# Optimization experiments

Measured on AMD Instinct MI355X. Metric: run time of the kernel, lower is better.

The kernel has to match this reference:

```python
import jax, jax.numpy as jnp
import numpy as np

D_MODEL = 1024
N_HEADS = 16
HEAD_DIM = D_MODEL // N_HEADS
NEG = -10000.0  # module uses -10000, not -inf


def setup_inputs() -> dict:
    key = jax.random.key(0)
    ks = jax.random.split(key, 8)
    B, T = 4, 2048
    q = jax.random.normal(ks[0], (B, T, D_MODEL), dtype=jnp.float32)
    k = jax.random.normal(ks[1], (B, T, D_MODEL), dtype=jnp.float32)
    v = jax.random.normal(ks[2], (B, T, D_MODEL), dtype=jnp.float32)
    attn_mask = jnp.ones((B, T), dtype=jnp.float32)
    # xavier_uniform for square [d, d] weights: limit = sqrt(6/(d+d))
    lim = float(np.sqrt(6.0 / (D_MODEL + D_MODEL)))
    Wq = jax.random.uniform(ks[3], (D_MODEL, D_MODEL), jnp.float32, -lim, lim)
    Wk = jax.random.uniform(ks[4], (D_MODEL, D_MODEL), jnp.float32, -lim, lim)
    Wv = jax.random.uniform(ks[5], (D_MODEL, D_MODEL), jnp.float32, -lim, lim)
    Wo = jax.random.uniform(ks[6], (D_MODEL, D_MODEL), jnp.float32, -lim, lim)
    return {"q": q, "k": k, "v": v, "attn_mask": attn_mask,
            "Wq": Wq, "Wk": Wk, "Wv": Wv, "Wo": Wo, "mask_future": 1}


def _split_heads(x):
    B, T, _ = x.shape
    return x.reshape(B, T, N_HEADS, HEAD_DIM).transpose(0, 2, 1, 3)  # [B,H,T,D]


def reference(q, k, v, attn_mask, Wq, Wk, Wv, Wo, mask_future):
    # torch Linear: y = x @ W.T  (weights stored [out, in])
    qh = _split_heads(jnp.einsum('btd,ed->bte', q, Wq))
    kh = _split_heads(jnp.einsum('btd,ed->bte', k, Wk))
    vh = _split_heads(jnp.einsum('btd,ed->bte', v, Wv))
    L, S = qh.shape[-2], kh.shape[-2]
    # dual scale: each of q and k scaled by 1/d**0.25
    scale = 1.0 / jnp.sqrt(jnp.sqrt(jnp.float32(HEAD_DIM)))
    scores = jnp.einsum('bhld,bhsd->bhls', qh * scale, kh * scale)
    if mask_future:
        causal_bias = jnp.triu(jnp.full((L, S), NEG, dtype=scores.dtype), k=1)
        scores = scores + causal_bias
    # padding mask: attn_mask [B, S] -> broadcast [B,1,1,S]; 0 entries -> -10000
    pad = attn_mask[:, None, None, :]
    scores = jnp.where(pad == 0, jnp.asarray(NEG, scores.dtype), scores)
    probs = jax.nn.softmax(scores, axis=-1)  # dropout p=0.0 -> identity
    ctx = jnp.einsum('bhls,bhsd->bhld', probs, vh)
    B = ctx.shape[0]
    ctx = ctx.transpose(0, 2, 1, 3).reshape(B, L, D_MODEL)
    return jnp.einsum('btd,ed->bte', ctx, Wo)
```

## Files before the change

kernel.cpp:

```cpp
#include <hip/hip_runtime.h>

typedef unsigned short u16;
typedef __attribute__((ext_vector_type(8))) _Float16 f16x8;
typedef __attribute__((ext_vector_type(2))) __fp16 fp16v2;
typedef __attribute__((ext_vector_type(4))) float f32x4;
typedef __attribute__((ext_vector_type(16))) float f32x16;

#define T_SEQ 2048
#define NH 16
#define DH 64
#define DM 1024
#define NEG2 (-14426.95f)
#define QS2 (0.42466089f)

__device__ __forceinline__ unsigned pk2(float a, float b) {
  union { fp16v2 v; unsigned u; } c;
  c.v = __builtin_amdgcn_cvt_pkrtz(a, b);
  return c.u;
}
__device__ __forceinline__ u16 f2h(float a) {
  union { _Float16 h; u16 u; } c; c.h = (_Float16)a; return c.u;
}

__device__ __forceinline__ void async_load16(const void* g, void* l) {
  __builtin_amdgcn_global_load_lds(
      (const __attribute__((address_space(1))) unsigned int*)(g),
      (__attribute__((address_space(3))) unsigned int*)(l), 16, 0, 0);
}

__global__ __launch_bounds__(256) void convert_all(
    const float* __restrict__ q, const float* __restrict__ k, const float* __restrict__ v,
    const float* __restrict__ Wq, const float* __restrict__ Wk, const float* __restrict__ Wv,
    const float* __restrict__ Wo, u16* __restrict__ xb, u16* __restrict__ wb) {
  int blk = blockIdx.x;
  const float* src; u16* dst;
  if (blk < 12288) {
    int s = blk >> 12;
    src = (s == 0) ? q : (s == 1) ? k : v;
    dst = xb + (size_t)s * 8388608u;
    blk &= 4095;
  } else {
    int s = (blk - 12288) >> 9;
    src = (s == 0) ? Wq : (s == 1) ? Wk : (s == 2) ? Wv : Wo;
    dst = wb + (size_t)s * 1048576u;
    blk = (blk - 12288) & 511;
  }
  size_t base = (size_t)blk * 2048 + (size_t)threadIdx.x * 8;
  float4 a = *(const float4*)(src + base);
  float4 b2 = *(const float4*)(src + base + 4);
  uint4 st;
  st.x = pk2(a.x, a.y); st.y = pk2(a.z, a.w);
  st.z = pk2(b2.x, b2.y); st.w = pk2(b2.z, b2.w);
  *(uint4*)(dst + base) = st;
}

__global__ __launch_bounds__(256) void gemm_qkv(const u16* __restrict__ A,
                                                const u16* __restrict__ Wqb,
                                                const u16* __restrict__ Wkb,
                                                const u16* __restrict__ Wvb,
                                                u16* __restrict__ Qh, u16* __restrict__ Kh,
                                                u16* __restrict__ VTh) {
  __shared__ char lds[33792];
  const int tid = threadIdx.x;
  const int wid = tid >> 6, lane = tid & 63;
  const int l32 = lane & 31, lh = lane >> 5;
  const int m0 = blockIdx.x * 128;
  const int n0 = blockIdx.y * 128;
  const int which = n0 >> 10;
  const int n0l = n0 & 1023;
  const u16* As = A + (size_t)which * 8388608u;
  const u16* Bw = (which == 0) ? Wqb : (which == 1) ? Wkb : Wvb;
  const int wm = wid >> 1, wn = wid & 1;
  f32x16 acc[2][2] = {};

  const u16* gA = As + (size_t)(m0 + wid * 32 + l32) * 1024 + lh * 8;
  const u16* gB = Bw + (size_t)(n0l + wid * 32 + l32) * 1024 + lh * 8;
  async_load16(gA, lds + (wid * 2 + 0) * 1024);
  async_load16(gA + 16, lds + (wid * 2 + 1) * 1024);
  async_load16(gB, lds + 8192 + (wid * 2 + 0) * 1024);
  async_load16(gB + 16, lds + 8192 + (wid * 2 + 1) * 1024);

  for (int it = 0; it < 32; ++it) {
    __syncthreads();
    char* cur = lds + (it & 1) * 16384;
    if (it < 31) {
      char* nxt = lds + ((it + 1) & 1) * 16384;
      int kt = (it + 1) * 32;
      async_load16(gA + kt, nxt + (wid * 2 + 0) * 1024);
      async_load16(gA + kt + 16, nxt + (wid * 2 + 1) * 1024);
      async_load16(gB + kt, nxt + 8192 + (wid * 2 + 0) * 1024);
      async_load16(gB + kt + 16, nxt + 8192 + (wid * 2 + 1) * 1024);
    }
    char* const rb = (which < 2) ? (cur + 8192) : cur;
    char* const cb = (which < 2) ? cur : (cur + 8192);
    for (int ks = 0; ks < 2; ++ks) {
      f16x8 rf[2], cf[2];
      for (int i = 0; i < 2; ++i) {
        rf[i] = *(const f16x8*)(rb + ((wm * 2 + i) * 2 + ks) * 1024 + lane * 16);
        cf[i] = *(const f16x8*)(cb + ((wn * 2 + i) * 2 + ks) * 1024 + lane * 16);
      }
      for (int i = 0; i < 2; ++i)
        for (int j = 0; j < 2; ++j)
          acc[i][j] = __builtin_amdgcn_mfma_f32_32x32x16_f16(rf[i], cf[j], acc[i][j], 0, 0, 0);
    }
  }

  const float s = (which < 2) ? QS2 : 1.0f;
  __syncthreads();
  for (int i = 0; i < 2; ++i)
    for (int j = 0; j < 2; ++j) {
      int colb = wn * 64 + j * 32 + l32;
      int rowb = wm * 64 + i * 32 + 4 * lh;
      for (int g = 0; g < 4; ++g) {
        uint2 pv;
        pv.x = pk2(acc[i][j][4 * g + 0] * s, acc[i][j][4 * g + 1] * s);
        pv.y = pk2(acc[i][j][4 * g + 2] * s, acc[i][j][4 * g + 3] * s);
        *(uint2*)(lds + colb * 264 + (rowb + 8 * g) * 2) = pv;
      }
    }
  __syncthreads();

  const int b = m0 >> 11, t0 = m0 & 2047, h0 = n0l >> 6;
  if (which < 2) {
    u16* O = which ? Kh : Qh;
    for (int p = 0; p < 8; ++p) {
      int row = p * 16 + (tid >> 4);
      int seg = tid & 15;
      uint4 val = *(const uint4*)(lds + row * 264 + seg * 16);
      int hl = seg >> 3, dh0 = (seg & 7) * 8;
      *(uint4*)(O + (((size_t)(b * NH + h0 + hl) * T_SEQ + t0 + row) << 6) + dh0) = val;
    }
  } else {
    for (int p = 0; p < 8; ++p) {
      int row = p * 16 + (tid >> 4);
      int seg = tid & 15;
      uint4 val = *(const uint4*)(lds + row * 264 + seg * 16);
      int h = h0 + (row >> 6), dh = row & 63;
      *(uint4*)(VTh + (((size_t)(b * NH + h) * DH + dh) << 11) + t0 + seg * 8) = val;
    }
  }
}

__global__ __launch_bounds__(256) void gemm_out(const u16* __restrict__ A,
                                                const u16* __restrict__ Bw,
                                                float* __restrict__ O) {
  __shared__ char lds[32768];
  const int tid = threadIdx.x;
  const int wid = tid >> 6, lane = tid & 63;
  const int l32 = lane & 31, lh = lane >> 5;
  const int m0 = blockIdx.x * 128, n0 = blockIdx.y * 128;
  const int wm = wid >> 1, wn = wid & 1;
  f32x16 acc[2][2] = {};

  const u16* gA = A + (size_t)(m0 + wid * 32 + l32) * 1024 + lh * 8;
  const u16* gB = Bw + (size_t)(n0 + wid * 32 + l32) * 1024 + lh * 8;
  async_load16(gA, lds + (wid * 2 + 0) * 1024);
  async_load16(gA + 16, lds + (wid * 2 + 1) * 1024);
  async_load16(gB, lds + 8192 + (wid * 2 + 0) * 1024);
  async_load16(gB + 16, lds + 8192 + (wid * 2 + 1) * 1024);

  for (int it = 0; it < 32; ++it) {
    __syncthreads();
    char* cur = lds + (it & 1) * 16384;
    if (it < 31) {
      char* nxt = lds + ((it + 1) & 1) * 16384;
      int kt = (it + 1) * 32;
      async_load16(gA + kt, nxt + (wid * 2 + 0) * 1024);
      async_load16(gA + kt + 16, nxt + (wid * 2 + 1) * 1024);
      async_load16(gB + kt, nxt + 8192 + (wid * 2 + 0) * 1024);
      async_load16(gB + kt + 16, nxt + 8192 + (wid * 2 + 1) * 1024);
    }
    for (int ks = 0; ks < 2; ++ks) {
      f16x8 af[2], bf[2];
      for (int i = 0; i < 2; ++i) {
        af[i] = *(const f16x8*)(cur + ((wm * 2 + i) * 2 + ks) * 1024 + lane * 16);
        bf[i] = *(const f16x8*)(cur + 8192 + ((wn * 2 + i) * 2 + ks) * 1024 + lane * 16);
      }
      for (int i = 0; i < 2; ++i)
        for (int j = 0; j < 2; ++j)
          acc[i][j] = __builtin_amdgcn_mfma_f32_32x32x16_f16(af[i], bf[j], acc[i][j], 0, 0, 0);
    }
  }
  for (int i = 0; i < 2; ++i)
    for (int j = 0; j < 2; ++j) {
      int col = n0 + wn * 64 + j * 32 + l32;
      int rowb = m0 + wm * 64 + i * 32 + 4 * lh;
      for (int g = 0; g < 4; ++g)
        for (int rr = 0; rr < 4; ++rr)
          O[(size_t)(rowb + 8 * g + rr) * 1024 + col] = acc[i][j][4 * g + rr];
    }
}

__global__ __launch_bounds__(512) void attn_kernel(const u16* __restrict__ Qh,
                                                   const u16* __restrict__ Kh,
                                                   const u16* __restrict__ VTh,
                                                   const float* __restrict__ attn_mask,
                                                   const int* __restrict__ mfp,
                                                   u16* __restrict__ ctx) {
  __shared__ char kls[8192];
  __shared__ char vls[8192];
  __shared__ char pls[8][2048];
  __shared__ float maskb[T_SEQ];
  __shared__ int mzf;

  const int tid = threadIdx.x;
  const int wid = tid >> 6, lane = tid & 63;
  const int lm = lane & 15, lq = lane >> 4;
  const int bid = blockIdx.x;
  const int bh_i = bid & 63, p8 = bid >> 6;
  const int b = bh_i >> 4, h = bh_i & 15;
  const int mf = *mfp;
  const size_t bh = (size_t)(b * NH + h);
  const u16* Qbh = Qh + bh * T_SEQ * DH;
  const u16* Kbh = Kh + bh * T_SEQ * DH;
  const u16* VTbh = VTh + bh * DH * T_SEQ;

  if (tid == 0) mzf = 0;
  __syncthreads();
  {
    int az = 0;
    for (int i = tid; i < T_SEQ; i += 512) {
      float mv = attn_mask[(size_t)b * T_SEQ + i];
      maskb[i] = (mv == 0.0f) ? NEG2 : 0.0f;
      az |= (mv == 0.0f);
    }
    if (az) mzf = 1;
  }
  __syncthreads();
  const int maskzero = mzf;

  for (int half = 0; half < 2; ++half) {
    const int qt = half ? (15 - p8) : p8;
    const int q0 = qt * 128;
    const int qw = q0 + wid * 16;
    f16x8 qf[2];
    qf[0] = *(const f16x8*)(Qbh + (size_t)(qw + lm) * DH + lq * 8);
    qf[1] = *(const f16x8*)(Qbh + (size_t)(qw + lm) * DH + 32 + lq * 8);

    f32x4 acc[4] = {};
    float mprev = -1e30f, lsum = 0.f;

    const int nch = mf ? (qt + 1) * 2 : 32;
    for (int c = 0; c < nch; ++c) {
      const int s0 = c * 64;
      __syncthreads();
      async_load16(Kbh + (size_t)(s0 + (wid >> 1) * 16 + lm) * DH + (wid & 1) * 32 + lq * 8,
                   kls + wid * 1024);
      async_load16(VTbh + (size_t)((wid >> 1) * 16 + lm) * T_SEQ + s0 + (wid & 1) * 32 + lq * 8,
                   vls + wid * 1024);
      __syncthreads();

      f32x4 sc[4];
      for (int st = 0; st < 4; ++st) {
        f32x4 z = {0.f, 0.f, 0.f, 0.f};
        sc[st] = z;
        for (int kk = 0; kk < 2; ++kk) {
          f16x8 kf = *(const f16x8*)(kls + ((st * 2 + kk) * 64 + lane) * 16);
          sc[st] = __builtin_amdgcn_mfma_f32_16x16x32_f16(kf, qf[kk], sc[st], 0, 0, 0);
        }
      }
      if (maskzero) {
        for (int st = 0; st < 4; ++st) {
          f32x4 mb = *(const f32x4*)(maskb + s0 + st * 16 + lq * 4);
          for (int r = 0; r < 4; ++r) sc[st][r] += mb[r];
        }
      }
      if (mf && (s0 + 64 > qw)) {
        int qg = qw + lm;
        for (int st = 0; st < 4; ++st)
          for (int r = 0; r < 4; ++r)
            if (s0 + st * 16 + lq * 4 + r > qg) sc[st][r] = NEG2;
      }
      float mx = fmaxf(fmaxf(sc[0][0], sc[0][1]), fmaxf(sc[0][2], sc[0][3]));
      for (int st = 1; st < 4; ++st) {
        float t2 = fmaxf(fmaxf(sc[st][0], sc[st][1]), fmaxf(sc[st][2], sc[st][3]));
        mx = fmaxf(mx, t2);
      }
      mx = fmaxf(mx, __shfl_xor(mx, 16));
      mx = fmaxf(mx, __shfl_xor(mx, 32));
      float mn = mprev;
      if (__ballot(mx > mprev) != 0ull) {
        mn = fmaxf(mprev, mx);
        float alpha = exp2f(mprev - mn);
        for (int r = 0; r < 4; ++r) {
          float ar = __shfl(alpha, lq * 4 + r);
          for (int nt = 0; nt < 4; ++nt) acc[nt][r] *= ar;
        }
        lsum *= alpha;
        mprev = mn;
      }
      float ps = 0.f;
      for (int st = 0; st < 4; ++st)
        for (int r = 0; r < 4; ++r) {
          float p = exp2f(sc[st][r] - mn);
          sc[st][r] = p;
          ps += p;
        }
      ps += __shfl_xor(ps, 16);
      ps += __shfl_xor(ps, 32);
      lsum += ps;
      {
        char* pw = pls[wid];
        for (int st = 0; st < 4; ++st) {
          int kk = st >> 1;
          int lqp = (st & 1) * 2 + (lq >> 1);
          uint2 pv;
          pv.x = pk2(sc[st][0], sc[st][1]);
          pv.y = pk2(sc[st][2], sc[st][3]);
          *(uint2*)(pw + kk * 1024 + (lqp * 16 + lm) * 16 + (lq & 1) * 8) = pv;
        }
      }
      asm volatile("s_waitcnt lgkmcnt(0)" ::: "memory");
      for (int kk = 0; kk < 2; ++kk) {
        f16x8 pf = *(const f16x8*)(pls[wid] + kk * 1024 + lane * 16);
        for (int nt = 0; nt < 4; ++nt) {
          f16x8 vf = *(const f16x8*)(vls + ((nt * 2 + kk) * 64 + lane) * 16);
          acc[nt] = __builtin_amdgcn_mfma_f32_16x16x32_f16(pf, vf, acc[nt], 0, 0, 0);
        }
      }
    }
    float inv = 1.0f / lsum;
    for (int r = 0; r < 4; ++r) {
      float ir = __shfl(inv, lq * 4 + r);
      int t = qw + lq * 4 + r;
      for (int nt = 0; nt < 4; ++nt)
        ctx[((size_t)(b * T_SEQ + t) * DM) + h * DH + nt * 16 + lm] = f2h(acc[nt][r] * ir);
    }
  }
}

extern "C" void kernel_launch(void* const* d_in, const int* in_sizes, int n_in,
                              void* d_out, int out_size, void* d_ws, size_t ws_size,
                              hipStream_t stream) {
  const float* q = (const float*)d_in[0];
  const float* k = (const float*)d_in[1];
  const float* v = (const float*)d_in[2];
  const float* attn_mask = (const float*)d_in[3];
  const float* Wq = (const float*)d_in[4];
  const float* Wk = (const float*)d_in[5];
  const float* Wv = (const float*)d_in[6];
  const float* Wo = (const float*)d_in[7];
  const int* mf = (const int*)d_in[8];

  u16* ws = (u16*)d_ws;
  u16* qb  = ws;
  u16* wqb = ws + 3u * 8388608u;
  u16* wkb = wqb + 1048576u;
  u16* wvb = wkb + 1048576u;
  u16* wob = wvb + 1048576u;
  u16* Qh  = wob + 1048576u;
  u16* Kh  = Qh + 8388608u;
  u16* VTh = Kh + 8388608u;
  u16* ctxb = ws;

  convert_all<<<14336, 256, 0, stream>>>(q, k, v, Wq, Wk, Wv, Wo, qb, wqb);

  dim3 gq(64, 24);
  gemm_qkv<<<gq, 256, 0, stream>>>(qb, wqb, wkb, wvb, Qh, Kh, VTh);

  attn_kernel<<<512, 512, 0, stream>>>(Qh, Kh, VTh, attn_mask, mf, ctxb);

  dim3 gg(64, 8);
  gemm_out<<<gg, 256, 0, stream>>>(ctxb, wob, (float*)d_out);
}
```

Before: 375.9 us.

## Fuse fp32-to-fp16 conversion into GEMM loads and register-prefetch attention tiles

Removes the separate conversion kernel. The QKV and output GEMMs now load fp32 inputs and weights straight from global memory, convert them in registers and store fp16 into double-buffered LDS, replacing the async global-to-LDS loads with register-staged prefetch. The attention kernel gains double-buffered K/V tiles with register prefetch, which removes one barrier per chunk, and stores the padding mask as fp16. This avoids writing and re-reading the fp16 copies of the inputs, but the GEMMs read twice as many bytes per tile, and each weight tile is reconverted once per block that uses it.

```diff
diff --git a/kernel.cpp b/kernel.cpp
--- a/kernel.cpp
+++ b/kernel.cpp
@@ -22,44 +22,10 @@
   union { _Float16 h; u16 u; } c; c.h = (_Float16)a; return c.u;
 }
 
-__device__ __forceinline__ void async_load16(const void* g, void* l) {
-  __builtin_amdgcn_global_load_lds(
-      (const __attribute__((address_space(1))) unsigned int*)(g),
-      (__attribute__((address_space(3))) unsigned int*)(l), 16, 0, 0);
-}
-
-__global__ __launch_bounds__(256) void convert_all(
-    const float* __restrict__ q, const float* __restrict__ k, const float* __restrict__ v,
-    const float* __restrict__ Wq, const float* __restrict__ Wk, const float* __restrict__ Wv,
-    const float* __restrict__ Wo, u16* __restrict__ xb, u16* __restrict__ wb) {
-  int blk = blockIdx.x;
-  const float* src; u16* dst;
-  if (blk < 12288) {
-    int s = blk >> 12;
-    src = (s == 0) ? q : (s == 1) ? k : v;
-    dst = xb + (size_t)s * 8388608u;
-    blk &= 4095;
-  } else {
-    int s = (blk - 12288) >> 9;
-    src = (s == 0) ? Wq : (s == 1) ? Wk : (s == 2) ? Wv : Wo;
-    dst = wb + (size_t)s * 1048576u;
-    blk = (blk - 12288) & 511;
-  }
-  size_t base = (size_t)blk * 2048 + (size_t)threadIdx.x * 8;
-  float4 a = *(const float4*)(src + base);
-  float4 b2 = *(const float4*)(src + base + 4);
-  uint4 st;
-  st.x = pk2(a.x, a.y); st.y = pk2(a.z, a.w);
-  st.z = pk2(b2.x, b2.y); st.w = pk2(b2.z, b2.w);
-  *(uint4*)(dst + base) = st;
-}
-
-__global__ __launch_bounds__(256) void gemm_qkv(const u16* __restrict__ A,
-                                                const u16* __restrict__ Wqb,
-                                                const u16* __restrict__ Wkb,
-                                                const u16* __restrict__ Wvb,
-                                                u16* __restrict__ Qh, u16* __restrict__ Kh,
-                                                u16* __restrict__ VTh) {
+__global__ __launch_bounds__(256) void gemm_qkv(
+    const float* __restrict__ Xq, const float* __restrict__ Xk, const float* __restrict__ Xv,
+    const float* __restrict__ Wqf, const float* __restrict__ Wkf, const float* __restrict__ Wvf,
+    u16* __restrict__ Qh, u16* __restrict__ Kh, u16* __restrict__ VTh) {
   __shared__ char lds[33792];
   const int tid = threadIdx.x;
   const int wid = tid >> 6, lane = tid & 63;
@@ -68,29 +34,41 @@
   const int n0 = blockIdx.y * 128;
   const int which = n0 >> 10;
   const int n0l = n0 & 1023;
-  const u16* As = A + (size_t)which * 8388608u;
-  const u16* Bw = (which == 0) ? Wqb : (which == 1) ? Wkb : Wvb;
+  const float* Xs = (which == 0) ? Xq : (which == 1) ? Xk : Xv;
+  const float* Wf = (which == 0) ? Wqf : (which == 1) ? Wkf : Wvf;
   const int wm = wid >> 1, wn = wid & 1;
   f32x16 acc[2][2] = {};
 
-  const u16* gA = As + (size_t)(m0 + wid * 32 + l32) * 1024 + lh * 8;
-  const u16* gB = Bw + (size_t)(n0l + wid * 32 + l32) * 1024 + lh * 8;
-  async_load16(gA, lds + (wid * 2 + 0) * 1024);
-  async_load16(gA + 16, lds + (wid * 2 + 1) * 1024);
-  async_load16(gB, lds + 8192 + (wid * 2 + 0) * 1024);
-  async_load16(gB + 16, lds + 8192 + (wid * 2 + 1) * 1024);
+  const float* gA = Xs + (size_t)(m0 + wid * 32 + l32) * 1024 + lh * 8;
+  const float* gB = Wf + (size_t)(n0l + wid * 32 + l32) * 1024 + lh * 8;
+
+  {
+    float4 a0 = *(const float4*)(gA), a1 = *(const float4*)(gA + 4);
+    float4 a2 = *(const float4*)(gA + 16), a3 = *(const float4*)(gA + 20);
+    float4 b0 = *(const float4*)(gB), b1 = *(const float4*)(gB + 4);
+    float4 b2 = *(const float4*)(gB + 16), b3 = *(const float4*)(gB + 20);
+    uint4 p;
+    p.x = pk2(a0.x, a0.y); p.y = pk2(a0.z, a0.w); p.z = pk2(a1.x, a1.y); p.w = pk2(a1.z, a1.w);
+    *(uint4*)(lds + (wid * 2 + 0) * 1024 + lane * 16) = p;
+    p.x = pk2(a2.x, a2.y); p.y = pk2(a2.z, a2.w); p.z = pk2(a3.x, a3.y); p.w = pk2(a3.z, a3.w);
+    *(uint4*)(lds + (wid * 2 + 1) * 1024 + lane * 16) = p;
+    p.x = pk2(b0.x, b0.y); p.y = pk2(b0.z, b0.w); p.z = pk2(b1.x, b1.y); p.w = pk2(b1.z, b1.w);
+    *(uint4*)(lds + 8192 + (wid * 2 + 0) * 1024 + lane * 16) = p;
+    p.x = pk2(b2.x, b2.y); p.y = pk2(b2.z, b2.w); p.z = pk2(b3.x, b3.y); p.w = pk2(b3.z, b3.w);
+    *(uint4*)(lds + 8192 + (wid * 2 + 1) * 1024 + lane * 16) = p;
+  }
 
   for (int it = 0; it < 32; ++it) {
+    float4 a0, a1, a2, a3, b0, b1, b2, b3;
+    if (it < 31) {
+      int kt = (it + 1) * 32;
+      a0 = *(const float4*)(gA + kt);      a1 = *(const float4*)(gA + kt + 4);
+      a2 = *(const float4*)(gA + kt + 16); a3 = *(const float4*)(gA + kt + 20);
+      b0 = *(const float4*)(gB + kt);      b1 = *(const float4*)(gB + kt + 4);
+      b2 = *(const float4*)(gB + kt + 16); b3 = *(const float4*)(gB + kt + 20);
+    }
     __syncthreads();
-    char* cur = lds + (it & 1) * 16384;
-    if (it < 31) {
-      char* nxt = lds + ((it + 1) & 1) * 16384;
-      int kt = (it + 1) * 32;
-      async_load16(gA + kt, nxt + (wid * 2 + 0) * 1024);
-      async_load16(gA + kt + 16, nxt + (wid * 2 + 1) * 1024);
-      async_load16(gB + kt, nxt + 8192 + (wid * 2 + 0) * 1024);
-      async_load16(gB + kt + 16, nxt + 8192 + (wid * 2 + 1) * 1024);
-    }
+    char* cur = lds + ((it & 1) << 14);
     char* const rb = (which < 2) ? (cur + 8192) : cur;
     char* const cb = (which < 2) ? cur : (cur + 8192);
     for (int ks = 0; ks < 2; ++ks) {
@@ -102,6 +80,18 @@
       for (int i = 0; i < 2; ++i)
         for (int j = 0; j < 2; ++j)
           acc[i][j] = __builtin_amdgcn_mfma_f32_32x32x16_f16(rf[i], cf[j], acc[i][j], 0, 0, 0);
+    }
+    if (it < 31) {
+      char* nxt = lds + (((it + 1) & 1) << 14);
+      uint4 p;
+      p.x = pk2(a0.x, a0.y); p.y = pk2(a0.z, a0.w); p.z = pk2(a1.x, a1.y); p.w = pk2(a1.z, a1.w);
+      *(uint4*)(nxt + (wid * 2 + 0) * 1024 + lane * 16) = p;
+      p.x = pk2(a2.x, a2.y); p.y = pk2(a2.z, a2.w); p.z = pk2(a3.x, a3.y); p.w = pk2(a3.z, a3.w);
+      *(uint4*)(nxt + (wid * 2 + 1) * 1024 + lane * 16) = p;
+      p.x = pk2(b0.x, b0.y); p.y = pk2(b0.z, b0.w); p.z = pk2(b1.x, b1.y); p.w = pk2(b1.z, b1.w);
+      *(uint4*)(nxt + 8192 + (wid * 2 + 0) * 1024 + lane * 16) = p;
+      p.x = pk2(b2.x, b2.y); p.y = pk2(b2.z, b2.w); p.z = pk2(b3.x, b3.y); p.w = pk2(b3.z, b3.w);
+      *(uint4*)(nxt + 8192 + (wid * 2 + 1) * 1024 + lane * 16) = p;
     }
   }
 
@@ -142,7 +132,7 @@
 }
 
 __global__ __launch_bounds__(256) void gemm_out(const u16* __restrict__ A,
-                                                const u16* __restrict__ Bw,
+                                                const float* __restrict__ WoF,
                                                 float* __restrict__ O) {
   __shared__ char lds[32768];
   const int tid = threadIdx.x;
@@ -153,23 +143,32 @@
   f32x16 acc[2][2] = {};
 
   const u16* gA = A + (size_t)(m0 + wid * 32 + l32) * 1024 + lh * 8;
-  const u16* gB = Bw + (size_t)(n0 + wid * 32 + l32) * 1024 + lh * 8;
-  async_load16(gA, lds + (wid * 2 + 0) * 1024);
-  async_load16(gA + 16, lds + (wid * 2 + 1) * 1024);
-  async_load16(gB, lds + 8192 + (wid * 2 + 0) * 1024);
-  async_load16(gB + 16, lds + 8192 + (wid * 2 + 1) * 1024);
+  const float* gB = WoF + (size_t)(n0 + wid * 32 + l32) * 1024 + lh * 8;
+
+  {
+    uint4 qa0 = *(const uint4*)(gA), qa1 = *(const uint4*)(gA + 16);
+    float4 b0 = *(const float4*)(gB), b1 = *(const float4*)(gB + 4);
+    float4 b2 = *(const float4*)(gB + 16), b3 = *(const float4*)(gB + 20);
+    *(uint4*)(lds + (wid * 2 + 0) * 1024 + lane * 16) = qa0;
+    *(uint4*)(lds + (wid * 2 + 1) * 1024 + lane * 16) = qa1;
+    uint4 p;
+    p.x = pk2(b0.x, b0.y); p.y = pk2(b0.z, b0.w); p.z = pk2(b1.x, b1.y); p.w = pk2(b1.z, b1.w);
+    *(uint4*)(lds + 8192 + (wid * 2 + 0) * 1024 + lane * 16) = p;
+    p.x = pk2(b2.x, b2.y); p.y = pk2(b2.z, b2.w); p.z = pk2(b3.x, b3.y); p.w = pk2(b3.z, b3.w);
+    *(uint4*)(lds + 8192 + (wid * 2 + 1) * 1024 + lane * 16) = p;
+  }
 
   for (int it = 0; it < 32; ++it) {
+    uint4 qa0, qa1;
+    float4 b0, b1, b2, b3;
+    if (it < 31) {
+      int kt = (it + 1) * 32;
+      qa0 = *(const uint4*)(gA + kt); qa1 = *(const uint4*)(gA + kt + 16);
+      b0 = *(const float4*)(gB + kt);      b1 = *(const float4*)(gB + kt + 4);
+      b2 = *(const float4*)(gB + kt + 16); b3 = *(const float4*)(gB + kt + 20);
+    }
     __syncthreads();
-    char* cur = lds + (it & 1) * 16384;
-    if (it < 31) {
-      char* nxt = lds + ((it + 1) & 1) * 16384;
-      int kt = (it + 1) * 32;
-      async_load16(gA + kt, nxt + (wid * 2 + 0) * 1024);
-      async_load16(gA + kt + 16, nxt + (wid * 2 + 1) * 1024);
-      async_load16(gB + kt, nxt + 8192 + (wid * 2 + 0) * 1024);
-      async_load16(gB + kt + 16, nxt + 8192 + (wid * 2 + 1) * 1024);
-    }
+    char* cur = lds + ((it & 1) << 14);
     for (int ks = 0; ks < 2; ++ks) {
       f16x8 af[2], bf[2];
       for (int i = 0; i < 2; ++i) {
@@ -179,6 +178,16 @@
       for (int i = 0; i < 2; ++i)
         for (int j = 0; j < 2; ++j)
           acc[i][j] = __builtin_amdgcn_mfma_f32_32x32x16_f16(af[i], bf[j], acc[i][j], 0, 0, 0);
+    }
+    if (it < 31) {
+      char* nxt = lds + (((it + 1) & 1) << 14);
+      *(uint4*)(nxt + (wid * 2 + 0) * 1024 + lane * 16) = qa0;
+      *(uint4*)(nxt + (wid * 2 + 1) * 1024 + lane * 16) = qa1;
+      uint4 p;
+      p.x = pk2(b0.x, b0.y); p.y = pk2(b0.z, b0.w); p.z = pk2(b1.x, b1.y); p.w = pk2(b1.z, b1.w);
+      *(uint4*)(nxt + 8192 + (wid * 2 + 0) * 1024 + lane * 16) = p;
+      p.x = pk2(b2.x, b2.y); p.y = pk2(b2.z, b2.w); p.z = pk2(b3.x, b3.y); p.w = pk2(b3.z, b3.w);
+      *(uint4*)(nxt + 8192 + (wid * 2 + 1) * 1024 + lane * 16) = p;
     }
   }
   for (int i = 0; i < 2; ++i)
@@ -197,10 +206,10 @@
                                                    const float* __restrict__ attn_mask,
                                                    const int* __restrict__ mfp,
                                                    u16* __restrict__ ctx) {
-  __shared__ char kls[8192];
-  __shared__ char vls[8192];
+  __shared__ char kls[2][8192];
+  __shared__ char vls[2][8192];
   __shared__ char pls[8][2048];
-  __shared__ float maskb[T_SEQ];
+  __shared__ u16 maskb[T_SEQ];
   __shared__ int mzf;
 
   const int tid = threadIdx.x;
@@ -221,13 +230,15 @@
     int az = 0;
     for (int i = tid; i < T_SEQ; i += 512) {
       float mv = attn_mask[(size_t)b * T_SEQ + i];
-      maskb[i] = (mv == 0.0f) ? NEG2 : 0.0f;
+      maskb[i] = f2h((mv == 0.0f) ? NEG2 : 0.0f);
       az |= (mv == 0.0f);
     }
     if (az) mzf = 1;
   }
   __syncthreads();
   const int maskzero = mzf;
+
+  const int krow = (wid >> 1) * 16 + lm, koff = (wid & 1) * 32 + lq * 8;
 
   for (int half = 0; half < 2; ++half) {
     const int qt = half ? (15 - p8) : p8;
@@ -241,28 +252,37 @@
     float mprev = -1e30f, lsum = 0.f;
 
     const int nch = mf ? (qt + 1) * 2 : 32;
+    uint4 kv = *(const uint4*)(Kbh + (size_t)(0 + krow) * DH + koff);
+    uint4 vv = *(const uint4*)(VTbh + (size_t)krow * T_SEQ + 0 + koff);
+    __syncthreads();
+    *(uint4*)(kls[0] + wid * 1024 + lane * 16) = kv;
+    *(uint4*)(vls[0] + wid * 1024 + lane * 16) = vv;
+
     for (int c = 0; c < nch; ++c) {
       const int s0 = c * 64;
+      if (c + 1 < nch) {
+        int s1 = s0 + 64;
+        kv = *(const uint4*)(Kbh + (size_t)(s1 + krow) * DH + koff);
+        vv = *(const uint4*)(VTbh + (size_t)krow * T_SEQ + s1 + koff);
+      }
       __syncthreads();
-      async_load16(Kbh + (size_t)(s0 + (wid >> 1) * 16 + lm) * DH + (wid & 1) * 32 + lq * 8,
-                   kls + wid * 1024);
-      async_load16(VTbh + (size_t)((wid >> 1) * 16 + lm) * T_SEQ + s0 + (wid & 1) * 32 + lq * 8,
-                   vls + wid * 1024);
-      __syncthreads();
+      const char* kb = kls[c & 1];
+      const char* vb = vls[c & 1];
 
       f32x4 sc[4];
       for (int st = 0; st < 4; ++st) {
         f32x4 z = {0.f, 0.f, 0.f, 0.f};
         sc[st] = z;
         for (int kk = 0; kk < 2; ++kk) {
-          f16x8 kf = *(const f16x8*)(kls + ((st * 2 + kk) * 64 + lane) * 16);
+          f16x8 kf = *(const f16x8*)(kb + ((st * 2 + kk) * 64 + lane) * 16);
           sc[st] = __builtin_amdgcn_mfma_f32_16x16x32_f16(kf, qf[kk], sc[st], 0, 0, 0);
         }
       }
       if (maskzero) {
         for (int st = 0; st < 4; ++st) {
-          f32x4 mb = *(const f32x4*)(maskb + s0 + st * 16 + lq * 4);
-          for (int r = 0; r < 4; ++r) sc[st][r] += mb[r];
+          uint2 mraw = *(const uint2*)(maskb + s0 + st * 16 + lq * 4);
+          const _Float16* mh = (const _Float16*)&mraw;
+          for (int r = 0; r < 4; ++r) sc[st][r] += (float)mh[r];
         }
       }
       if (mf && (s0 + 64 > qw)) {
@@ -314,9 +334,13 @@
       for (int kk = 0; kk < 2; ++kk) {
         f16x8 pf = *(const f16x8*)(pls[wid] + kk * 1024 + lane * 16);
         for (int nt = 0; nt < 4; ++nt) {
-          f16x8 vf = *(const f16x8*)(vls + ((nt * 2 + kk) * 64 + lane) * 16);
+          f16x8 vf = *(const f16x8*)(vb + ((nt * 2 + kk) * 64 + lane) * 16);
           acc[nt] = __builtin_amdgcn_mfma_f32_16x16x32_f16(pf, vf, acc[nt], 0, 0, 0);
         }
+      }
+      if (c + 1 < nch) {
+        *(uint4*)(kls[(c + 1) & 1] + wid * 1024 + lane * 16) = kv;
+        *(uint4*)(vls[(c + 1) & 1] + wid * 1024 + lane * 16) = vv;
       }
     }
     float inv = 1.0f / lsum;
@@ -343,23 +367,16 @@
   const int* mf = (const int*)d_in[8];
 
   u16* ws = (u16*)d_ws;
-  u16* qb  = ws;
-  u16* wqb = ws + 3u * 8388608u;
-  u16* wkb = wqb + 1048576u;
-  u16* wvb = wkb + 1048576u;
-  u16* wob = wvb + 1048576u;
-  u16* Qh  = wob + 1048576u;
+  u16* ctxb = ws;
+  u16* Qh  = ws + 8388608u;
   u16* Kh  = Qh + 8388608u;
   u16* VTh = Kh + 8388608u;
-  u16* ctxb = ws;
-
-  convert_all<<<14336, 256, 0, stream>>>(q, k, v, Wq, Wk, Wv, Wo, qb, wqb);
 
   dim3 gq(64, 24);
-  gemm_qkv<<<gq, 256, 0, stream>>>(qb, wqb, wkb, wvb, Qh, Kh, VTh);
+  gemm_qkv<<<gq, 256, 0, stream>>>(q, k, v, Wq, Wk, Wv, Qh, Kh, VTh);
 
   attn_kernel<<<512, 512, 0, stream>>>(Qh, Kh, VTh, attn_mask, mf, ctxb);
 
   dim3 gg(64, 8);
-  gemm_out<<<gg, 256, 0, stream>>>(ctxb, wob, (float*)d_out);
-}
+  gemm_out<<<gg, 256, 0, stream>>>(ctxb, Wo, (float*)d_out);
+}
```

Result: slower. 427.3 us (+13.7%).

## Triple-buffer GEMM LDS stages and register-prefetch K/V in attention

Applied to the files above, without the earlier changes.

Both GEMM kernels move from double-buffered LDS with two __syncthreads per step to a three-stage ring. They issue loads two steps ahead and use vmcnt-based waits plus a single s_barrier per step, so more global-load latency is hidden behind the MFMA work. The attention kernel replaces its synchronous async K/V LDS loads with register prefetch two chunks ahead into double-buffered LDS, leaving one barrier per chunk, and stores the padding mask as fp16 to shrink LDS. The cost is more LDS per block (48 KB per GEMM block, and larger attention LDS), which may lower occupancy, and the hand-written waitcnt logic is more fragile.

```diff
diff --git a/kernel.cpp b/kernel.cpp
--- a/kernel.cpp
+++ b/kernel.cpp
@@ -26,6 +26,10 @@
   __builtin_amdgcn_global_load_lds(
       (const __attribute__((address_space(1))) unsigned int*)(g),
       (__attribute__((address_space(3))) unsigned int*)(l), 16, 0, 0);
+}
+
+__device__ __forceinline__ void lgkm_barrier() {
+  asm volatile("s_waitcnt lgkmcnt(0)\n\ts_barrier" ::: "memory");
 }
 
 __global__ __launch_bounds__(256) void convert_all(
@@ -60,7 +64,7 @@
                                                 const u16* __restrict__ Wvb,
                                                 u16* __restrict__ Qh, u16* __restrict__ Kh,
                                                 u16* __restrict__ VTh) {
-  __shared__ char lds[33792];
+  __shared__ char lds[49152];
   const int tid = threadIdx.x;
   const int wid = tid >> 6, lane = tid & 63;
   const int l32 = lane & 31, lh = lane >> 5;
@@ -75,22 +79,27 @@
 
   const u16* gA = As + (size_t)(m0 + wid * 32 + l32) * 1024 + lh * 8;
   const u16* gB = Bw + (size_t)(n0l + wid * 32 + l32) * 1024 + lh * 8;
-  async_load16(gA, lds + (wid * 2 + 0) * 1024);
-  async_load16(gA + 16, lds + (wid * 2 + 1) * 1024);
-  async_load16(gB, lds + 8192 + (wid * 2 + 0) * 1024);
-  async_load16(gB + 16, lds + 8192 + (wid * 2 + 1) * 1024);
+
+#define STAGE(it2, buf)                                                   \
+  do {                                                                    \
+    int kt_ = (it2) * 32;                                                 \
+    async_load16(gA + kt_, (buf) + (wid * 2 + 0) * 1024);                 \
+    async_load16(gA + kt_ + 16, (buf) + (wid * 2 + 1) * 1024);            \
+    async_load16(gB + kt_, (buf) + 8192 + (wid * 2 + 0) * 1024);          \
+    async_load16(gB + kt_ + 16, (buf) + 8192 + (wid * 2 + 1) * 1024);     \
+  } while (0)
+
+  STAGE(0, lds);
+  STAGE(1, lds + 16384);
 
   for (int it = 0; it < 32; ++it) {
-    __syncthreads();
-    char* cur = lds + (it & 1) * 16384;
-    if (it < 31) {
-      char* nxt = lds + ((it + 1) & 1) * 16384;
-      int kt = (it + 1) * 32;
-      async_load16(gA + kt, nxt + (wid * 2 + 0) * 1024);
-      async_load16(gA + kt + 16, nxt + (wid * 2 + 1) * 1024);
-      async_load16(gB + kt, nxt + 8192 + (wid * 2 + 0) * 1024);
-      async_load16(gB + kt + 16, nxt + 8192 + (wid * 2 + 1) * 1024);
-    }
+    if (it == 31)
+      asm volatile("s_waitcnt vmcnt(0)" ::: "memory");
+    else
+      asm volatile("s_waitcnt vmcnt(4)" ::: "memory");
+    asm volatile("s_barrier" ::: "memory");
+    char* cur = lds + (it % 3) * 16384;
+    if (it + 2 < 32) STAGE(it + 2, lds + ((it + 2) % 3) * 16384);
     char* const rb = (which < 2) ? (cur + 8192) : cur;
     char* const cb = (which < 2) ? cur : (cur + 8192);
     for (int ks = 0; ks < 2; ++ks) {
@@ -104,6 +113,7 @@
           acc[i][j] = __builtin_amdgcn_mfma_f32_32x32x16_f16(rf[i], cf[j], acc[i][j], 0, 0, 0);
     }
   }
+#undef STAGE
 
   const float s = (which < 2) ? QS2 : 1.0f;
   __syncthreads();
@@ -144,7 +154,7 @@
 __global__ __launch_bounds__(256) void gemm_out(const u16* __restrict__ A,
                                                 const u16* __restrict__ Bw,
                                                 float* __restrict__ O) {
-  __shared__ char lds[32768];
+  __shared__ char lds[49152];
   const int tid = threadIdx.x;
   const int wid = tid >> 6, lane = tid & 63;
   const int l32 = lane & 31, lh = lane >> 5;
@@ -154,22 +164,27 @@
 
   const u16* gA = A + (size_t)(m0 + wid * 32 + l32) * 1024 + lh * 8;
   const u16* gB = Bw + (size_t)(n0 + wid * 32 + l32) * 1024 + lh * 8;
-  async_load16(gA, lds + (wid * 2 + 0) * 1024);
-  async_load16(gA + 16, lds + (wid * 2 + 1) * 1024);
-  async_load16(gB, lds + 8192 + (wid * 2 + 0) * 1024);
-  async_load16(gB + 16, lds + 8192 + (wid * 2 + 1) * 1024);
+
+#define STAGE(it2, buf)                                                   \
+  do {                                                                    \
+    int kt_ = (it2) * 32;                                                 \
+    async_load16(gA + kt_, (buf) + (wid * 2 + 0) * 1024);                 \
+    async_load16(gA + kt_ + 16, (buf) + (wid * 2 + 1) * 1024);            \
+    async_load16(gB + kt_, (buf) + 8192 + (wid * 2 + 0) * 1024);          \
+    async_load16(gB + kt_ + 16, (buf) + 8192 + (wid * 2 + 1) * 1024);     \
+  } while (0)
+
+  STAGE(0, lds);
+  STAGE(1, lds + 16384);
 
   for (int it = 0; it < 32; ++it) {
-    __syncthreads();
-    char* cur = lds + (it & 1) * 16384;
-    if (it < 31) {
-      char* nxt = lds + ((it + 1) & 1) * 16384;
-      int kt = (it + 1) * 32;
-      async_load16(gA + kt, nxt + (wid * 2 + 0) * 1024);
-      async_load16(gA + kt + 16, nxt + (wid * 2 + 1) * 1024);
-      async_load16(gB + kt, nxt + 8192 + (wid * 2 + 0) * 1024);
-      async_load16(gB + kt + 16, nxt + 8192 + (wid * 2 + 1) * 1024);
-    }
+    if (it == 31)
+      asm volatile("s_waitcnt vmcnt(0)" ::: "memory");
+    else
+      asm volatile("s_waitcnt vmcnt(4)" ::: "memory");
+    asm volatile("s_barrier" ::: "memory");
+    char* cur = lds + (it % 3) * 16384;
+    if (it + 2 < 32) STAGE(it + 2, lds + ((it + 2) % 3) * 16384);
     for (int ks = 0; ks < 2; ++ks) {
       f16x8 af[2], bf[2];
       for (int i = 0; i < 2; ++i) {
@@ -181,6 +196,8 @@
           acc[i][j] = __builtin_amdgcn_mfma_f32_32x32x16_f16(af[i], bf[j], acc[i][j], 0, 0, 0);
     }
   }
+#undef STAGE
+
   for (int i = 0; i < 2; ++i)
     for (int j = 0; j < 2; ++j) {
       int col = n0 + wn * 64 + j * 32 + l32;
@@ -197,10 +214,10 @@
                                                    const float* __restrict__ attn_mask,
                                                    const int* __restrict__ mfp,
                                                    u16* __restrict__ ctx) {
-  __shared__ char kls[8192];
-  __shared__ char vls[8192];
+  __shared__ char kls[2][8192];
+  __shared__ char vls[2][8192];
   __shared__ char pls[8][2048];
-  __shared__ float maskb[T_SEQ];
+  __shared__ u16 maskb[T_SEQ];
   __shared__ int mzf;
 
   const int tid = threadIdx.x;
@@ -221,13 +238,15 @@
     int az = 0;
     for (int i = tid; i < T_SEQ; i += 512) {
       float mv = attn_mask[(size_t)b * T_SEQ + i];
-      maskb[i] = (mv == 0.0f) ? NEG2 : 0.0f;
+      maskb[i] = f2h((mv == 0.0f) ? NEG2 : 0.0f);
       az |= (mv == 0.0f);
     }
     if (az) mzf = 1;
   }
   __syncthreads();
   const int maskzero = mzf;
+
+  const int krow = (wid >> 1) * 16 + lm, koff = (wid & 1) * 32 + lq * 8;
 
   for (int half = 0; half < 2; ++half) {
     const int qt = half ? (15 - p8) : p8;
@@ -241,28 +260,42 @@
     float mprev = -1e30f, lsum = 0.f;
 
     const int nch = mf ? (qt + 1) * 2 : 32;
+    uint4 kvr[2], vvr[2];
+    kvr[0] = *(const uint4*)(Kbh + (size_t)krow * DH + koff);
+    vvr[0] = *(const uint4*)(VTbh + (size_t)krow * T_SEQ + koff);
+    if (nch > 1) {
+      kvr[1] = *(const uint4*)(Kbh + (size_t)(64 + krow) * DH + koff);
+      vvr[1] = *(const uint4*)(VTbh + (size_t)krow * T_SEQ + 64 + koff);
+    }
+    lgkm_barrier();
+    *(uint4*)(kls[0] + wid * 1024 + lane * 16) = kvr[0];
+    *(uint4*)(vls[0] + wid * 1024 + lane * 16) = vvr[0];
+
     for (int c = 0; c < nch; ++c) {
       const int s0 = c * 64;
-      __syncthreads();
-      async_load16(Kbh + (size_t)(s0 + (wid >> 1) * 16 + lm) * DH + (wid & 1) * 32 + lq * 8,
-                   kls + wid * 1024);
-      async_load16(VTbh + (size_t)((wid >> 1) * 16 + lm) * T_SEQ + s0 + (wid & 1) * 32 + lq * 8,
-                   vls + wid * 1024);
-      __syncthreads();
+      if (c + 2 < nch) {
+        int s2 = s0 + 128;
+        kvr[c & 1] = *(const uint4*)(Kbh + (size_t)(s2 + krow) * DH + koff);
+        vvr[c & 1] = *(const uint4*)(VTbh + (size_t)krow * T_SEQ + s2 + koff);
+      }
+      lgkm_barrier();
+      const char* kb = kls[c & 1];
+      const char* vb = vls[c & 1];
 
       f32x4 sc[4];
       for (int st = 0; st < 4; ++st) {
         f32x4 z = {0.f, 0.f, 0.f, 0.f};
         sc[st] = z;
         for (int kk = 0; kk < 2; ++kk) {
-          f16x8 kf = *(const f16x8*)(kls + ((st * 2 + kk) * 64 + lane) * 16);
+          f16x8 kf = *(const f16x8*)(kb + ((st * 2 + kk) * 64 + lane) * 16);
           sc[st] = __builtin_amdgcn_mfma_f32_16x16x32_f16(kf, qf[kk], sc[st], 0, 0, 0);
         }
       }
       if (maskzero) {
         for (int st = 0; st < 4; ++st) {
-          f32x4 mb = *(const f32x4*)(maskb + s0 + st * 16 + lq * 4);
-          for (int r = 0; r < 4; ++r) sc[st][r] += mb[r];
+          uint2 mraw = *(const uint2*)(maskb + s0 + st * 16 + lq * 4);
+          const _Float16* mh = (const _Float16*)&mraw;
+          for (int r = 0; r < 4; ++r) sc[st][r] += (float)mh[r];
         }
       }
       if (mf && (s0 + 64 > qw)) {
@@ -314,9 +347,13 @@
       for (int kk = 0; kk < 2; ++kk) {
         f16x8 pf = *(const f16x8*)(pls[wid] + kk * 1024 + lane * 16);
         for (int nt = 0; nt < 4; ++nt) {
-          f16x8 vf = *(const f16x8*)(vls + ((nt * 2 + kk) * 64 + lane) * 16);
+          f16x8 vf = *(const f16x8*)(vb + ((nt * 2 + kk) * 64 + lane) * 16);
           acc[nt] = __builtin_amdgcn_mfma_f32_16x16x32_f16(pf, vf, acc[nt], 0, 0, 0);
         }
+      }
+      if (c + 1 < nch) {
+        *(uint4*)(kls[(c + 1) & 1] + wid * 1024 + lane * 16) = kvr[(c + 1) & 1];
+        *(uint4*)(vls[(c + 1) & 1] + wid * 1024 + lane * 16) = vvr[(c + 1) & 1];
       }
     }
     float inv = 1.0f / lsum;
```

After: 394.1 us. 1.05x slower.
